# Optimization experiments

Hardware: AMD Instinct MI355X
Metric: run time of the kernel (lower is better)

The kernel has to match this reference:

```python
import jax, jax.numpy as jnp
import numpy as np

B, D, T = 16, 64, 256
BD = TD = H = 128
H2 = H // 2
NRES = 2


def setup_inputs() -> dict:
    key = jax.random.key(0)
    ks = jax.random.split(key, 24)
    r = lambda i, shape, s=0.05: jax.random.normal(ks[i], shape, jnp.float32) * s
    return {
        "branch_emb": jax.random.normal(ks[0], (B, D, BD), jnp.float32),
        "trunk_emb": jax.random.normal(ks[1], (B, T, TD), jnp.float32),
        "mask": jnp.ones((B, D), jnp.float32),
        "W_bil": r(2, (H, BD, TD)),
        "b_bil": r(3, (H,)),
        "W_br": r(4, (H, BD)), "b_br": r(5, (H,)),
        "W_tr": r(6, (H, TD)), "b_tr": r(7, (H,)),
        "g_fn": jnp.ones((H,), jnp.float32), "beta_fn": jnp.zeros((H,), jnp.float32),
        "res_w1": r(8, (NRES, H, H)), "res_b1": r(9, (NRES, H)),
        "res_w2": r(10, (NRES, H, H)), "res_b2": r(11, (NRES, H)),
        "res_g": jnp.ones((NRES, H), jnp.float32), "res_beta": jnp.zeros((NRES, H), jnp.float32),
        "pos_w1": r(12, (H2, H)), "pos_b1": r(13, (H2,)),
        "pos_w2": r(14, (1, H2)), "pos_b2": r(15, (1,)),
        "ex_w1": r(16, (H2, H)), "ex_b1": r(17, (H2,)),
        "ex_w2": r(18, (1, H2)), "ex_b2": r(19, (1,)),
    }


def _layer_norm(x, g, b, eps=1e-5):
    m = jnp.mean(x, axis=-1, keepdims=True)
    v = jnp.mean((x - m) ** 2, axis=-1, keepdims=True)
    return (x - m) * jax.lax.rsqrt(v + eps) * g + b


def reference(branch_emb, trunk_emb, mask, W_bil, b_bil, W_br, b_br, W_tr, b_tr,
              g_fn, beta_fn, res_w1, res_b1, res_w2, res_b2, res_g, res_beta,
              pos_w1, pos_b1, pos_w2, pos_b2, ex_w1, ex_b1, ex_w2, ex_b2):
    # Bilinear decomposition: never materialize the (B*D*T, dim) expanded inputs.
    # nn.Bilinear: out_h = x1 @ W[h] @ x2 + b[h]
    tmp = jnp.einsum('bdi,hij->bdhj', branch_emb, W_bil)          # (B,D,H,TD)
    fused = jnp.einsum('bdhj,btj->bdth', tmp, trunk_emb) + b_bil  # (B,D,T,H)
    fused = fused \
        + (branch_emb @ W_br.T + b_br)[:, :, None, :] \
        + (trunk_emb @ W_tr.T + b_tr)[:, None, :, :]
    fused = _layer_norm(fused, g_fn, beta_fn)
    for i in range(res_w1.shape[0]):
        h = jax.nn.gelu(fused @ res_w1[i].T + res_b1[i], approximate=False)
        h = h @ res_w2[i].T + res_b2[i]
        fused = _layer_norm(fused + h, res_g[i], res_beta[i])
    pos = jax.nn.gelu(fused @ pos_w1.T + pos_b1, approximate=False) @ pos_w2.T + pos_b2
    positions = jnp.clip(pos[..., 0], 0.0, 1.0)                   # (B,D,T)
    ex = jax.nn.gelu(fused @ ex_w1.T + ex_b1, approximate=False) @ ex_w2.T + ex_b2
    existence = jax.nn.sigmoid(ex[..., 0])                        # (B,D,T)
    m = mask[:, :, None]
    return positions * m, existence * m
```

## Files before the change

kernel.cpp:

```cpp
#include <hip/hip_runtime.h>
#include <hip/hip_bf16.h>

#define BDT_TOT 262144

typedef __attribute__((ext_vector_type(8))) short bf16x8;
typedef __attribute__((ext_vector_type(4))) float f32x4;

__device__ __forceinline__ unsigned short f2b(float f) {
  __hip_bfloat16 h = __float2bfloat16(f);
  return *reinterpret_cast<unsigned short*>(&h);
}
__device__ __forceinline__ float bu2f(unsigned u16) {
  union { unsigned u; float f; } c;
  c.u = u16 << 16;
  return c.f;
}
__device__ __forceinline__ float gelu_f(float x) {
  float x2 = x * x;
  float t = 1.5957691216057308f * x * fmaf(0.044715f, x2, 1.0f);
  return x * __builtin_amdgcn_rcpf(1.0f + __expf(-t));
}

__device__ __forceinline__ void stage_f32(unsigned char* dst, const float* __restrict__ src,
                                          int ld, int tid, int nch, int nthr) {
  for (int c = tid; c < nch; c += nthr) {
    int row = c >> 4, kc = c & 15;
    const float* s = src + row * ld + kc * 8;
    float4 u = *(const float4*)(s);
    float4 v = *(const float4*)(s + 4);
    union { unsigned short h[8]; uint4 q; } pk;
    pk.h[0] = f2b(u.x); pk.h[1] = f2b(u.y); pk.h[2] = f2b(u.z); pk.h[3] = f2b(u.w);
    pk.h[4] = f2b(v.x); pk.h[5] = f2b(v.y); pk.h[6] = f2b(v.z); pk.h[7] = f2b(v.w);
    *(uint4*)(dst + row * 256 + ((kc * 16) ^ ((row & 7) << 4))) = pk.q;
  }
}

__device__ __forceinline__ void stage_bf16(unsigned char* dst, const unsigned short* __restrict__ src,
                                           int tid, int nch, int nthr) {
  for (int c = tid; c < nch; c += nthr) {
    int row = c >> 4, kc = c & 15;
    uint4 q = *(const uint4*)(src + row * 128 + kc * 8);
    *(uint4*)(dst + row * 256 + ((kc * 16) ^ ((row & 7) << 4))) = q;
  }
}


__device__ __forceinline__ void gemm_tile(const unsigned char* Ar, const unsigned char* Br,
                                          int lane, int wm, int wn, f32x4 acc[4][2]) {
  const int lr = lane & 15, lk = lane >> 4;
#pragma unroll
  for (int ks = 0; ks < 4; ++ks) {
    const int kb = ks * 64 + lk * 16;
    bf16x8 a[4], bb[2];
#pragma unroll
    for (int mf = 0; mf < 4; ++mf) {
      int m = wm * 64 + mf * 16 + lr;
      a[mf] = *(const bf16x8*)(Ar + m * 256 + (kb ^ ((m & 7) << 4)));
    }
#pragma unroll
    for (int nf = 0; nf < 2; ++nf) {
      int n = wn * 32 + nf * 16 + lr;
      bb[nf] = *(const bf16x8*)(Br + n * 256 + (kb ^ ((n & 7) << 4)));
    }
#pragma unroll
    for (int mf = 0; mf < 4; ++mf)
#pragma unroll
      for (int nf = 0; nf < 2; ++nf)
        acc[mf][nf] = __builtin_amdgcn_mfma_f32_16x16x32_bf16(a[mf], bb[nf], acc[mf][nf], 0, 0, 0);
  }
}

__device__ __forceinline__ void gemm_tile64(const unsigned char* Ar, const unsigned char* Br,
                                            int lane, int wn, f32x4 acc[4][2]) {
  const int lr = lane & 15, lk = lane >> 4;
#pragma unroll
  for (int ks = 0; ks < 4; ++ks) {
    const int kb = ks * 64 + lk * 16;
    bf16x8 a[4], bb[2];
#pragma unroll
    for (int mf = 0; mf < 4; ++mf) {
      int m = mf * 16 + lr;
      a[mf] = *(const bf16x8*)(Ar + m * 256 + (kb ^ ((m & 7) << 4)));
    }
#pragma unroll
    for (int nf = 0; nf < 2; ++nf) {
      int n = wn * 32 + nf * 16 + lr;
      bb[nf] = *(const bf16x8*)(Br + n * 256 + (kb ^ ((n & 7) << 4)));
    }
#pragma unroll
    for (int mf = 0; mf < 4; ++mf)
#pragma unroll
      for (int nf = 0; nf < 2; ++nf)
        acc[mf][nf] = __builtin_amdgcn_mfma_f32_16x16x32_bf16(a[mf], bb[nf], acc[mf][nf], 0, 0, 0);
  }
}

__device__ __forceinline__ void zero_acc(f32x4 acc[4][2]) {
#pragma unroll
  for (int mf = 0; mf < 4; ++mf)
#pragma unroll
    for (int nf = 0; nf < 2; ++nf)
#pragma unroll
      for (int r = 0; r < 4; ++r) acc[mf][nf][r] = 0.0f;
}

__global__ __launch_bounds__(128) void rowlin_kernel(const float* __restrict__ in,
                                                     const float* __restrict__ W,
                                                     const float* __restrict__ b0,
                                                     const float* __restrict__ b1,
                                                     const float* __restrict__ b2,
                                                     float* __restrict__ out) {
  int r = blockIdx.x, h = threadIdx.x;
  __shared__ float xr[128];
  xr[h] = in[r * 128 + h];
  __syncthreads();
  const float* w = W + h * 128;
  float a = b0[h] + b1[h] + b2[h];
#pragma unroll 4
  for (int k = 0; k < 128; ++k) a = fmaf(xr[k], w[k], a);
  out[r * 128 + h] = a;
}

__global__ __launch_bounds__(256) void k_prep_cvt(
    const float* __restrict__ res_w1, const float* __restrict__ res_w2,
    const float* __restrict__ pos_w1, const float* __restrict__ ex_w1,
    unsigned short* __restrict__ wTb) {
  const int blk = blockIdx.x;
  const float* src; const float* src2 = nullptr;
  if (blk == 0)      src = res_w1;
  else if (blk == 1) src = res_w2;
  else if (blk == 2) src = res_w1 + 16384;
  else if (blk == 3) src = res_w2 + 16384;
  else               { src = pos_w1; src2 = ex_w1; }
  unsigned short* dst = wTb + blk * 16384;
  for (int c = threadIdx.x; c < 2048; c += 256) {
    const int row = c >> 4, kc = c & 15;
    const float* s = (src2 && row >= 64) ? (src2 + (row - 64) * 128 + kc * 8)
                                         : (src + row * 128 + kc * 8);
    float4 u = *(const float4*)s;
    float4 v = *(const float4*)(s + 4);
    union { unsigned short h[8]; uint4 q; } pk;
    pk.h[0]=f2b(u.x); pk.h[1]=f2b(u.y); pk.h[2]=f2b(u.z); pk.h[3]=f2b(u.w);
    pk.h[4]=f2b(v.x); pk.h[5]=f2b(v.y); pk.h[6]=f2b(v.z); pk.h[7]=f2b(v.w);
    *(uint4*)(dst + row * 128 + kc * 8) = pk.q;
  }
}

struct SMemTmp {
  unsigned char A[32768];
  unsigned char Bt[32768];
};

__global__ __launch_bounds__(512, 2) void k_tmp(const float* __restrict__ be,
                                                const float* __restrict__ Wb,
                                                const float* __restrict__ W_tr,
                                                unsigned short* __restrict__ tmp) {
  __shared__ SMemTmp sm;
  const int h = blockIdx.x >> 3, bd0 = (blockIdx.x & 7) << 7;
  const int tid = threadIdx.x, lane = tid & 63, w = tid >> 6, wm = w >> 2, wn = w & 3;
  const int lr = lane & 15, lk = lane >> 4;

  stage_f32(sm.A, be + bd0 * 128, 128, tid, 2048, 512);
  {
    const float* src = Wb + h * 16384;
    for (int it = tid; it < 4096; it += 512) {
      int i = it >> 5, j0 = (it & 31) * 4;
      float4 u = *(const float4*)(src + i * 128 + j0);
      float vv[4] = {u.x, u.y, u.z, u.w};
#pragma unroll
      for (int e = 0; e < 4; ++e) {
        int j = j0 + e;
        *(unsigned short*)(sm.Bt + j * 256 + ((2 * i) ^ ((j & 7) << 4))) = f2b(vv[e]);
      }
    }
  }
  __syncthreads();
  f32x4 acc[4][2];
  zero_acc(acc);
  gemm_tile(sm.A, sm.Bt, lane, wm, wn, acc);
  __syncthreads();
  float wtrv[2];
#pragma unroll
  for (int nf = 0; nf < 2; ++nf)
    wtrv[nf] = W_tr[h * 128 + wn * 32 + nf * 16 + lr];
#pragma unroll
  for (int mf = 0; mf < 4; ++mf)
#pragma unroll
    for (int nf = 0; nf < 2; ++nf)
#pragma unroll
      for (int r = 0; r < 4; ++r) {
        int row = wm * 64 + mf * 16 + lk * 4 + r;
        int col = wn * 32 + nf * 16 + lr;
        *(unsigned short*)(sm.A + row * 256 + col * 2) = f2b(acc[mf][nf][r] + wtrv[nf]);
      }
  __syncthreads();
  {
    int row = tid >> 2, part = tid & 3;
    const uint4* s = (const uint4*)(sm.A + row * 256 + part * 64);
    uint4* g = (uint4*)(tmp + (size_t)(bd0 + row) * 16384 + h * 128 + part * 32);
    g[0] = s[0]; g[1] = s[1]; g[2] = s[2]; g[3] = s[3];
  }
}

struct SMemMain {
  unsigned char A[16384];
  unsigned char Bm[32768];
  float ssum[64 * 4];
  float ssq[64 * 4];
  float part[2][64][2];
};

__device__ __forceinline__ void ln_store64(float (&x)[4][2][4], unsigned (&xp)[4][4],
                                           float* ssum, float* ssq,
                                           int lane, int wn,
                                           const float* __restrict__ g, const float* __restrict__ be,
                                           unsigned char* Adst) {
  const int lr = lane & 15, lk = lane >> 4;
#pragma unroll
  for (int mf = 0; mf < 4; ++mf)
#pragma unroll
    for (int r = 0; r < 4; ++r) {
      float a = x[mf][0][r] + x[mf][1][r];
      float qq = x[mf][0][r] * x[mf][0][r] + x[mf][1][r] * x[mf][1][r];
#pragma unroll
      for (int m = 1; m < 16; m <<= 1) { a += __shfl_xor(a, m); qq += __shfl_xor(qq, m); }
      if (lr == 0) {
        int row = mf * 16 + lk * 4 + r;
        ssum[row * 4 + wn] = a;
        ssq[row * 4 + wn] = qq;
      }
    }
  __syncthreads();
  float gv[2], bv[2];
#pragma unroll
  for (int nf = 0; nf < 2; ++nf) {
    int col = wn * 32 + nf * 16 + lr;
    gv[nf] = g[col]; bv[nf] = be[col];
  }
#pragma unroll
  for (int mf = 0; mf < 4; ++mf)
#pragma unroll
    for (int r = 0; r < 4; ++r) {
      int row = mf * 16 + lk * 4 + r;
      float sum = ssum[row * 4 + 0] + ssum[row * 4 + 1] + ssum[row * 4 + 2] + ssum[row * 4 + 3];
      float sq  = ssq[row * 4 + 0] + ssq[row * 4 + 1] + ssq[row * 4 + 2] + ssq[row * 4 + 3];
      float mean = sum * 0.0078125f;
      float var  = sq * 0.0078125f - mean * mean;
      float rq = rsqrtf(var + 1e-5f);
      unsigned pk = 0;
#pragma unroll
      for (int nf = 0; nf < 2; ++nf) {
        int col = wn * 32 + nf * 16 + lr;
        float y = (x[mf][nf][r] - mean) * rq * gv[nf] + bv[nf];
        unsigned short us = f2b(y);
        pk |= ((unsigned)us) << (16 * nf);
        *(unsigned short*)(Adst + row * 256 + ((col * 2) ^ ((row & 7) << 4))) = us;
      }
      xp[mf][r] = pk;
    }
}

__global__ __launch_bounds__(256, 2) void k_main(
    const float* __restrict__ trunk, const unsigned short* __restrict__ tmp,
    const unsigned short* __restrict__ wTb,
    const float* __restrict__ br_all,
    const float* __restrict__ g_fn, const float* __restrict__ beta_fn,
    const float* __restrict__ res_b1, const float* __restrict__ res_b2,
    const float* __restrict__ res_g, const float* __restrict__ res_beta,
    const float* __restrict__ pos_b1, const float* __restrict__ pos_w2, const float* __restrict__ pos_b2,
    const float* __restrict__ ex_b1, const float* __restrict__ ex_w2, const float* __restrict__ ex_b2,
    const float* __restrict__ maskp, float* __restrict__ out) {
  __shared__ SMemMain sm;
  const int orig = blockIdx.x;
  const int gid = (orig & 7) * 512 + (orig >> 3);
  const int bd = gid >> 2, qt = gid & 3;
  const int b = bd >> 6, t0 = qt << 6;
  const int tid = threadIdx.x, lane = tid & 63, wn = tid >> 6;
  const int lr = lane & 15, lk = lane >> 4;

  stage_f32(sm.A, trunk + (size_t)(b * 256 + t0) * 128, 128, tid, 1024, 256);
  stage_bf16(sm.Bm, tmp + (size_t)bd * 16384, tid, 2048, 256);
  __syncthreads();
  f32x4 acc[4][2];
  zero_acc(acc);
  gemm_tile64(sm.A, sm.Bm, lane, wn, acc);

  unsigned xp[4][4];
  {
    float x[4][2][4];
#pragma unroll
    for (int nf = 0; nf < 2; ++nf) {
      int col = wn * 32 + nf * 16 + lr;
      float bb = br_all[bd * 128 + col];
#pragma unroll
      for (int mf = 0; mf < 4; ++mf)
#pragma unroll
        for (int r = 0; r < 4; ++r)
          x[mf][nf][r] = acc[mf][nf][r] + bb;
    }
    __syncthreads();
    ln_store64(x, xp, sm.ssum, sm.ssq, lane, wn, g_fn, beta_fn, sm.A);
  }

  for (int i = 0; i < 2; ++i) {
    stage_bf16(sm.Bm, wTb + (i * 2) * 16384, tid, 2048, 256);
    __syncthreads();
    zero_acc(acc);
    gemm_tile64(sm.A, sm.Bm, lane, wn, acc);
    __syncthreads();
#pragma unroll
    for (int nf = 0; nf < 2; ++nf) {
      int col = wn * 32 + nf * 16 + lr;
      float b1v = res_b1[i * 128 + col];
#pragma unroll
      for (int mf = 0; mf < 4; ++mf)
#pragma unroll
        for (int r = 0; r < 4; ++r) {
          int row = mf * 16 + lk * 4 + r;
          float hh = gelu_f(acc[mf][nf][r] + b1v);
          *(unsigned short*)(sm.A + row * 256 + ((col * 2) ^ ((row & 7) << 4))) = f2b(hh);
        }
    }
    stage_bf16(sm.Bm, wTb + (i * 2 + 1) * 16384, tid, 2048, 256);
    __syncthreads();
    zero_acc(acc);
    gemm_tile64(sm.A, sm.Bm, lane, wn, acc);
    __syncthreads();
    {
      float x[4][2][4];
#pragma unroll
      for (int nf = 0; nf < 2; ++nf) {
        int col = wn * 32 + nf * 16 + lr;
        float b2v = res_b2[i * 128 + col];
#pragma unroll
        for (int mf = 0; mf < 4; ++mf)
#pragma unroll
          for (int r = 0; r < 4; ++r)
            x[mf][nf][r] = bu2f((xp[mf][r] >> (16 * nf)) & 0xffffu) + acc[mf][nf][r] + b2v;
      }
      ln_store64(x, xp, sm.ssum, sm.ssq, lane, wn, res_g + i * 128, res_beta + i * 128, sm.A);
    }
  }

  stage_bf16(sm.Bm, wTb + 4 * 16384, tid, 2048, 256);
  __syncthreads();
  zero_acc(acc);
  gemm_tile64(sm.A, sm.Bm, lane, wn, acc);

  float s3[4][4];
#pragma unroll
  for (int mf = 0; mf < 4; ++mf)
#pragma unroll
    for (int r = 0; r < 4; ++r) s3[mf][r] = 0.0f;
#pragma unroll
  for (int nf = 0; nf < 2; ++nf) {
    int col = wn * 32 + nf * 16 + lr;
    float bias1 = (col < 64) ? pos_b1[col] : ex_b1[col - 64];
    float w2v = (col < 64) ? pos_w2[col] : ex_w2[col - 64];
#pragma unroll
    for (int mf = 0; mf < 4; ++mf)
#pragma unroll
      for (int r = 0; r < 4; ++r)
        s3[mf][r] += gelu_f(acc[mf][nf][r] + bias1) * w2v;
  }
#pragma unroll
  for (int mf = 0; mf < 4; ++mf)
#pragma unroll
    for (int r = 0; r < 4; ++r) {
      float a = s3[mf][r];
#pragma unroll
      for (int m = 1; m < 16; m <<= 1) a += __shfl_xor(a, m);
      s3[mf][r] = a;
    }
  if (lr == 0) {
#pragma unroll
    for (int mf = 0; mf < 4; ++mf)
#pragma unroll
      for (int r = 0; r < 4; ++r) {
        int row = mf * 16 + lk * 4 + r;
        sm.part[wn >> 1][row][wn & 1] = s3[mf][r];
      }
  }
  __syncthreads();
  if (tid < 128) {
    int row = tid >> 1, head = tid & 1;
    float v = sm.part[head][row][0] + sm.part[head][row][1];
    float mk = maskp[bd];
    int outr = bd * 256 + t0 + row;
    if (head == 0) {
      v += pos_b2[0];
      v = fminf(fmaxf(v, 0.0f), 1.0f);
      out[outr] = v * mk;
    } else {
      v += ex_b2[0];
      v = 1.0f / (1.0f + expf(-v));
      out[BDT_TOT + outr] = v * mk;
    }
  }
}

extern "C" void kernel_launch(void* const* d_in, const int* in_sizes, int n_in,
                              void* d_out, int out_size, void* d_ws, size_t ws_size,
                              hipStream_t stream) {
  const float* branch   = (const float*)d_in[0];
  const float* trunk    = (const float*)d_in[1];
  const float* mask     = (const float*)d_in[2];
  const float* W_bil    = (const float*)d_in[3];
  const float* b_bil    = (const float*)d_in[4];
  const float* W_br     = (const float*)d_in[5];
  const float* b_br     = (const float*)d_in[6];
  const float* W_tr     = (const float*)d_in[7];
  const float* b_tr     = (const float*)d_in[8];
  const float* g_fn     = (const float*)d_in[9];
  const float* beta_fn  = (const float*)d_in[10];
  const float* res_w1   = (const float*)d_in[11];
  const float* res_b1   = (const float*)d_in[12];
  const float* res_w2   = (const float*)d_in[13];
  const float* res_b2   = (const float*)d_in[14];
  const float* res_g    = (const float*)d_in[15];
  const float* res_beta = (const float*)d_in[16];
  const float* pos_w1   = (const float*)d_in[17];
  const float* pos_b1   = (const float*)d_in[18];
  const float* pos_w2   = (const float*)d_in[19];
  const float* pos_b2   = (const float*)d_in[20];
  const float* ex_w1    = (const float*)d_in[21];
  const float* ex_b1    = (const float*)d_in[22];
  const float* ex_w2    = (const float*)d_in[23];
  const float* ex_b2    = (const float*)d_in[24];
  float* out = (float*)d_out;

  unsigned char* wsb = (unsigned char*)d_ws;
  unsigned short* tmp = (unsigned short*)wsb;
  float* br_all       = (float*)(wsb + 33554432);
  unsigned short* wTb = (unsigned short*)(wsb + 34078720);

  hipLaunchKernelGGL(k_prep_cvt, dim3(5), dim3(256), 0, stream,
                     res_w1, res_w2, pos_w1, ex_w1, wTb);
  hipLaunchKernelGGL(rowlin_kernel, dim3(1024), dim3(128), 0, stream,
                     branch, W_br, b_br, b_bil, b_tr, br_all);
  hipLaunchKernelGGL(k_tmp, dim3(1024), dim3(512), 0, stream, branch, W_bil, W_tr, tmp);
  hipLaunchKernelGGL(k_main, dim3(4096), dim3(256), 0, stream,
                     trunk, tmp, wTb, br_all, g_fn, beta_fn,
                     res_b1, res_b2, res_g, res_beta,
                     pos_b1, pos_w2, pos_b2, ex_b1, ex_w2, ex_b2,
                     mask, out);
}
```

Measured before the change: 310.2 us.

## Register-prefetch next weight tile during GEMM and epilogue work

Replaces the synchronous global-to-LDS staging of each 128x128 bf16 weight matrix with a register prefetch. The next matrix is loaded into registers while the current GEMM and its epilogue run, then written to LDS after a barrier. This hides global load latency behind compute. In exchange it uses 32 extra VGPRs per thread for the prefetch buffer, which may lower occupancy or cause spills.

After: 385.4 us. 1.24x slower.

```diff
diff --git a/kernel.cpp b/kernel.cpp
--- a/kernel.cpp
+++ b/kernel.cpp
@@ -41,6 +41,25 @@
     int row = c >> 4, kc = c & 15;
     uint4 q = *(const uint4*)(src + row * 128 + kc * 8);
     *(uint4*)(dst + row * 256 + ((kc * 16) ^ ((row & 7) << 4))) = q;
+  }
+}
+
+struct PF { uint4 v[8]; };
+
+__device__ __forceinline__ void pf_load(PF& p, const unsigned short* __restrict__ src, int tid) {
+#pragma unroll
+  for (int k = 0; k < 8; ++k) {
+    const int c = tid + k * 256;
+    const int row = c >> 4, kc = c & 15;
+    p.v[k] = *(const uint4*)(src + row * 128 + kc * 8);
+  }
+}
+__device__ __forceinline__ void pf_store(const PF& p, unsigned char* dst, int tid) {
+#pragma unroll
+  for (int k = 0; k < 8; ++k) {
+    const int c = tid + k * 256;
+    const int row = c >> 4, kc = c & 15;
+    *(uint4*)(dst + row * 256 + ((kc * 16) ^ ((row & 7) << 4))) = p.v[k];
   }
 }
 
@@ -281,6 +300,8 @@
   stage_f32(sm.A, trunk + (size_t)(b * 256 + t0) * 128, 128, tid, 1024, 256);
   stage_bf16(sm.Bm, tmp + (size_t)bd * 16384, tid, 2048, 256);
   __syncthreads();
+  PF pf;
+  pf_load(pf, wTb, tid);
   f32x4 acc[4][2];
   zero_acc(acc);
   gemm_tile64(sm.A, sm.Bm, lane, wn, acc);
@@ -299,15 +320,18 @@
           x[mf][nf][r] = acc[mf][nf][r] + bb;
     }
     __syncthreads();
+    pf_store(pf, sm.Bm, tid);
+    pf_load(pf, wTb + 16384, tid);
     ln_store64(x, xp, sm.ssum, sm.ssq, lane, wn, g_fn, beta_fn, sm.A);
   }
+  __syncthreads();
 
   for (int i = 0; i < 2; ++i) {
-    stage_bf16(sm.Bm, wTb + (i * 2) * 16384, tid, 2048, 256);
-    __syncthreads();
     zero_acc(acc);
     gemm_tile64(sm.A, sm.Bm, lane, wn, acc);
     __syncthreads();
+    pf_store(pf, sm.Bm, tid);
+    pf_load(pf, wTb + (i == 0 ? 2 : 4) * 16384, tid);
 #pragma unroll
     for (int nf = 0; nf < 2; ++nf) {
       int col = wn * 32 + nf * 16 + lr;
@@ -321,11 +345,12 @@
           *(unsigned short*)(sm.A + row * 256 + ((col * 2) ^ ((row & 7) << 4))) = f2b(hh);
         }
     }
-    stage_bf16(sm.Bm, wTb + (i * 2 + 1) * 16384, tid, 2048, 256);
     __syncthreads();
     zero_acc(acc);
     gemm_tile64(sm.A, sm.Bm, lane, wn, acc);
     __syncthreads();
+    pf_store(pf, sm.Bm, tid);
+    if (i == 0) pf_load(pf, wTb + 3 * 16384, tid);
     {
       float x[4][2][4];
 #pragma unroll
@@ -338,12 +363,12 @@
           for (int r = 0; r < 4; ++r)
             x[mf][nf][r] = bu2f((xp[mf][r] >> (16 * nf)) & 0xffffu) + acc[mf][nf][r] + b2v;
       }
-      ln_store64(x, xp, sm.ssum, sm.ssq, lane, wn, res_g + i * 128, res_beta + i * 128, sm.A);
-    }
-  }
-
-  stage_bf16(sm.Bm, wTb + 4 * 16384, tid, 2048, 256);
-  __syncthreads();
+      ln_store64(x, xp, sm.ssum, sm.ssq, lane, wn,
+                 res_g + i * 128, res_beta + i * 128, sm.A);
+    }
+    __syncthreads();
+  }
+
   zero_acc(acc);
   gemm_tile64(sm.A, sm.Bm, lane, wn, acc);
 
```

## Process two 64-row tiles per block to reuse staged weights

Applied to the files above, without the earlier changes.

Each main-kernel block now handles 128 trunk positions as two 64-row A tiles instead of one. Every staged B tile (the bilinear tmp slice and each MLP weight) is used by two GEMMs, which halves the weight staging and global loads per output row. The weight load for the next layer is also staged right after the LayerNorm write, removing some barriers. In exchange each thread keeps twice the accumulators and activations in registers, which adds register pressure under launch_bounds(256,2), and there are half as many blocks.

Result: slower. 650.6 us (+109.7%).

```diff
diff --git a/kernel.cpp b/kernel.cpp
--- a/kernel.cpp
+++ b/kernel.cpp
@@ -203,18 +203,15 @@
 }
 
 struct SMemMain {
-  unsigned char A[16384];
+  unsigned char A[2][16384];
   unsigned char Bm[32768];
-  float ssum[64 * 4];
-  float ssq[64 * 4];
-  float part[2][64][2];
+  float ssum[2][256];
+  float ssq[2][256];
+  float part[2][2][64][2];
 };
 
-__device__ __forceinline__ void ln_store64(float (&x)[4][2][4], unsigned (&xp)[4][4],
-                                           float* ssum, float* ssq,
-                                           int lane, int wn,
-                                           const float* __restrict__ g, const float* __restrict__ be,
-                                           unsigned char* Adst) {
+__device__ __forceinline__ void ln_stats(const float (&x)[4][2][4], float* ssum, float* ssq,
+                                         int lane, int wn) {
   const int lr = lane & 15, lk = lane >> 4;
 #pragma unroll
   for (int mf = 0; mf < 4; ++mf)
@@ -230,7 +227,14 @@
         ssq[row * 4 + wn] = qq;
       }
     }
-  __syncthreads();
+}
+
+__device__ __forceinline__ void ln_norm(const float (&x)[4][2][4], unsigned (&xp)[4][4],
+                                        const float* ssum, const float* ssq,
+                                        int lane, int wn,
+                                        const float* __restrict__ g, const float* __restrict__ be,
+                                        unsigned char* Adst) {
+  const int lr = lane & 15, lk = lane >> 4;
   float gv[2], bv[2];
 #pragma unroll
   for (int nf = 0; nf < 2; ++nf) {
@@ -272,121 +276,126 @@
     const float* __restrict__ maskp, float* __restrict__ out) {
   __shared__ SMemMain sm;
   const int orig = blockIdx.x;
-  const int gid = (orig & 7) * 512 + (orig >> 3);
-  const int bd = gid >> 2, qt = gid & 3;
-  const int b = bd >> 6, t0 = qt << 6;
+  const int gid = (orig & 7) * 256 + (orig >> 3);
+  const int bd = gid >> 1, th = gid & 1;
+  const int b = bd >> 6, t0 = th << 7;
   const int tid = threadIdx.x, lane = tid & 63, wn = tid >> 6;
   const int lr = lane & 15, lk = lane >> 4;
 
-  stage_f32(sm.A, trunk + (size_t)(b * 256 + t0) * 128, 128, tid, 1024, 256);
+  stage_f32(sm.A[0], trunk + (size_t)(b * 256 + t0) * 128, 128, tid, 1024, 256);
+  stage_f32(sm.A[1], trunk + (size_t)(b * 256 + t0 + 64) * 128, 128, tid, 1024, 256);
   stage_bf16(sm.Bm, tmp + (size_t)bd * 16384, tid, 2048, 256);
   __syncthreads();
-  f32x4 acc[4][2];
-  zero_acc(acc);
-  gemm_tile64(sm.A, sm.Bm, lane, wn, acc);
-
-  unsigned xp[4][4];
+
+  f32x4 accA[4][2], accB[4][2];
+  float x0[4][2][4], x1[4][2][4];
+  unsigned xp0[4][4], xp1[4][4];
+  float bb[2];
+#pragma unroll
+  for (int nf = 0; nf < 2; ++nf) bb[nf] = br_all[bd * 128 + wn * 32 + nf * 16 + lr];
+
+  zero_acc(accA); gemm_tile64(sm.A[0], sm.Bm, lane, wn, accA);
+  zero_acc(accB); gemm_tile64(sm.A[1], sm.Bm, lane, wn, accB);
+#pragma unroll
+  for (int nf = 0; nf < 2; ++nf)
+#pragma unroll
+    for (int mf = 0; mf < 4; ++mf)
+#pragma unroll
+      for (int r = 0; r < 4; ++r) {
+        x0[mf][nf][r] = accA[mf][nf][r] + bb[nf];
+        x1[mf][nf][r] = accB[mf][nf][r] + bb[nf];
+      }
+  ln_stats(x0, sm.ssum[0], sm.ssq[0], lane, wn);
+  ln_stats(x1, sm.ssum[1], sm.ssq[1], lane, wn);
+  __syncthreads();
+  ln_norm(x0, xp0, sm.ssum[0], sm.ssq[0], lane, wn, g_fn, beta_fn, sm.A[0]);
+  ln_norm(x1, xp1, sm.ssum[1], sm.ssq[1], lane, wn, g_fn, beta_fn, sm.A[1]);
+  stage_bf16(sm.Bm, wTb, tid, 2048, 256);
+  __syncthreads();
+
+  for (int i = 0; i < 2; ++i) {
+    zero_acc(accA); gemm_tile64(sm.A[0], sm.Bm, lane, wn, accA);
+    zero_acc(accB); gemm_tile64(sm.A[1], sm.Bm, lane, wn, accB);
+    __syncthreads();
+    {
+      float b1v[2];
+#pragma unroll
+      for (int nf = 0; nf < 2; ++nf) b1v[nf] = res_b1[i * 128 + wn * 32 + nf * 16 + lr];
+#pragma unroll
+      for (int nf = 0; nf < 2; ++nf)
+#pragma unroll
+        for (int mf = 0; mf < 4; ++mf)
+#pragma unroll
+          for (int r = 0; r < 4; ++r) {
+            int row = mf * 16 + lk * 4 + r;
+            int cb = ((wn * 32 + nf * 16 + lr) * 2) ^ ((row & 7) << 4);
+            *(unsigned short*)(sm.A[0] + row * 256 + cb) = f2b(gelu_f(accA[mf][nf][r] + b1v[nf]));
+            *(unsigned short*)(sm.A[1] + row * 256 + cb) = f2b(gelu_f(accB[mf][nf][r] + b1v[nf]));
+          }
+    }
+    stage_bf16(sm.Bm, wTb + (i * 2 + 1) * 16384, tid, 2048, 256);
+    __syncthreads();
+    zero_acc(accA); gemm_tile64(sm.A[0], sm.Bm, lane, wn, accA);
+    zero_acc(accB); gemm_tile64(sm.A[1], sm.Bm, lane, wn, accB);
+    {
+      float b2v[2];
+#pragma unroll
+      for (int nf = 0; nf < 2; ++nf) b2v[nf] = res_b2[i * 128 + wn * 32 + nf * 16 + lr];
+#pragma unroll
+      for (int nf = 0; nf < 2; ++nf)
+#pragma unroll
+        for (int mf = 0; mf < 4; ++mf)
+#pragma unroll
+          for (int r = 0; r < 4; ++r) {
+            x0[mf][nf][r] = bu2f((xp0[mf][r] >> (16 * nf)) & 0xffffu) + accA[mf][nf][r] + b2v[nf];
+            x1[mf][nf][r] = bu2f((xp1[mf][r] >> (16 * nf)) & 0xffffu) + accB[mf][nf][r] + b2v[nf];
+          }
+    }
+    ln_stats(x0, sm.ssum[0], sm.ssq[0], lane, wn);
+    ln_stats(x1, sm.ssum[1], sm.ssq[1], lane, wn);
+    __syncthreads();
+    ln_norm(x0, xp0, sm.ssum[0], sm.ssq[0], lane, wn, res_g + i * 128, res_beta + i * 128, sm.A[0]);
+    ln_norm(x1, xp1, sm.ssum[1], sm.ssq[1], lane, wn, res_g + i * 128, res_beta + i * 128, sm.A[1]);
+    stage_bf16(sm.Bm, wTb + (i == 0 ? 2 : 4) * 16384, tid, 2048, 256);
+    __syncthreads();
+  }
+
+  zero_acc(accA); gemm_tile64(sm.A[0], sm.Bm, lane, wn, accA);
+  zero_acc(accB); gemm_tile64(sm.A[1], sm.Bm, lane, wn, accB);
+
   {
-    float x[4][2][4];
+    float bias1[2], w2v[2];
 #pragma unroll
     for (int nf = 0; nf < 2; ++nf) {
       int col = wn * 32 + nf * 16 + lr;
-      float bb = br_all[bd * 128 + col];
+      bias1[nf] = (col < 64) ? pos_b1[col] : ex_b1[col - 64];
+      w2v[nf] = (col < 64) ? pos_w2[col] : ex_w2[col - 64];
+    }
+#pragma unroll
+    for (int half = 0; half < 2; ++half) {
 #pragma unroll
       for (int mf = 0; mf < 4; ++mf)
 #pragma unroll
-        for (int r = 0; r < 4; ++r)
-          x[mf][nf][r] = acc[mf][nf][r] + bb;
-    }
-    __syncthreads();
-    ln_store64(x, xp, sm.ssum, sm.ssq, lane, wn, g_fn, beta_fn, sm.A);
-  }
-
-  for (int i = 0; i < 2; ++i) {
-    stage_bf16(sm.Bm, wTb + (i * 2) * 16384, tid, 2048, 256);
-    __syncthreads();
-    zero_acc(acc);
-    gemm_tile64(sm.A, sm.Bm, lane, wn, acc);
-    __syncthreads();
-#pragma unroll
-    for (int nf = 0; nf < 2; ++nf) {
-      int col = wn * 32 + nf * 16 + lr;
-      float b1v = res_b1[i * 128 + col];
-#pragma unroll
-      for (int mf = 0; mf < 4; ++mf)
-#pragma unroll
         for (int r = 0; r < 4; ++r) {
-          int row = mf * 16 + lk * 4 + r;
-          float hh = gelu_f(acc[mf][nf][r] + b1v);
-          *(unsigned short*)(sm.A + row * 256 + ((col * 2) ^ ((row & 7) << 4))) = f2b(hh);
+          const f32x4 (&ac)[4][2] = half ? accB : accA;
+          float a = gelu_f(ac[mf][0][r] + bias1[0]) * w2v[0]
+                  + gelu_f(ac[mf][1][r] + bias1[1]) * w2v[1];
+#pragma unroll
+          for (int m = 1; m < 16; m <<= 1) a += __shfl_xor(a, m);
+          if (lr == 0) {
+            int row = mf * 16 + lk * 4 + r;
+            sm.part[half][wn >> 1][row][wn & 1] = a;
+          }
         }
     }
-    stage_bf16(sm.Bm, wTb + (i * 2 + 1) * 16384, tid, 2048, 256);
-    __syncthreads();
-    zero_acc(acc);
-    gemm_tile64(sm.A, sm.Bm, lane, wn, acc);
-    __syncthreads();
-    {
-      float x[4][2][4];
-#pragma unroll
-      for (int nf = 0; nf < 2; ++nf) {
-        int col = wn * 32 + nf * 16 + lr;
-        float b2v = res_b2[i * 128 + col];
-#pragma unroll
-        for (int mf = 0; mf < 4; ++mf)
-#pragma unroll
-          for (int r = 0; r < 4; ++r)
-            x[mf][nf][r] = bu2f((xp[mf][r] >> (16 * nf)) & 0xffffu) + acc[mf][nf][r] + b2v;
-      }
-      ln_store64(x, xp, sm.ssum, sm.ssq, lane, wn, res_g + i * 128, res_beta + i * 128, sm.A);
-    }
-  }
-
-  stage_bf16(sm.Bm, wTb + 4 * 16384, tid, 2048, 256);
-  __syncthreads();
-  zero_acc(acc);
-  gemm_tile64(sm.A, sm.Bm, lane, wn, acc);
-
-  float s3[4][4];
-#pragma unroll
-  for (int mf = 0; mf < 4; ++mf)
-#pragma unroll
-    for (int r = 0; r < 4; ++r) s3[mf][r] = 0.0f;
-#pragma unroll
-  for (int nf = 0; nf < 2; ++nf) {
-    int col = wn * 32 + nf * 16 + lr;
-    float bias1 = (col < 64) ? pos_b1[col] : ex_b1[col - 64];
-    float w2v = (col < 64) ? pos_w2[col] : ex_w2[col - 64];
-#pragma unroll
-    for (int mf = 0; mf < 4; ++mf)
-#pragma unroll
-      for (int r = 0; r < 4; ++r)
-        s3[mf][r] += gelu_f(acc[mf][nf][r] + bias1) * w2v;
-  }
-#pragma unroll
-  for (int mf = 0; mf < 4; ++mf)
-#pragma unroll
-    for (int r = 0; r < 4; ++r) {
-      float a = s3[mf][r];
-#pragma unroll
-      for (int m = 1; m < 16; m <<= 1) a += __shfl_xor(a, m);
-      s3[mf][r] = a;
-    }
-  if (lr == 0) {
-#pragma unroll
-    for (int mf = 0; mf < 4; ++mf)
-#pragma unroll
-      for (int r = 0; r < 4; ++r) {
-        int row = mf * 16 + lk * 4 + r;
-        sm.part[wn >> 1][row][wn & 1] = s3[mf][r];
-      }
-  }
-  __syncthreads();
-  if (tid < 128) {
-    int row = tid >> 1, head = tid & 1;
-    float v = sm.part[head][row][0] + sm.part[head][row][1];
+  }
+  __syncthreads();
+  if (tid < 256) {
+    int rid = tid >> 1, head = tid & 1;
+    int half = rid >> 6, row = rid & 63;
+    float v = sm.part[half][head][row][0] + sm.part[half][head][row][1];
     float mk = maskp[bd];
-    int outr = bd * 256 + t0 + row;
+    int outr = bd * 256 + t0 + half * 64 + row;
     if (head == 0) {
       v += pos_b2[0];
       v = fminf(fmaxf(v, 0.0f), 1.0f);
@@ -439,7 +448,7 @@
   hipLaunchKernelGGL(rowlin_kernel, dim3(1024), dim3(128), 0, stream,
                      branch, W_br, b_br, b_bil, b_tr, br_all);
   hipLaunchKernelGGL(k_tmp, dim3(1024), dim3(512), 0, stream, branch, W_bil, W_tr, tmp);
-  hipLaunchKernelGGL(k_main, dim3(4096), dim3(256), 0, stream,
+  hipLaunchKernelGGL(k_main, dim3(2048), dim3(256), 0, stream,
                      trunk, tmp, wTb, br_all, g_fn, beta_fn,
                      res_b1, res_b2, res_g, res_beta,
                      pos_b1, pos_w2, pos_b2, ex_b1, ex_w2, ex_b2,
```
